# Kernel optimization log

Measured on AMD Instinct MI355X. Metric: run time of the kernel, lower is better.

The kernel has to match this reference:

```python
import jax, jax.numpy as jnp
import numpy as np
from math import pi

N = 20000        # nodes
E = 640000       # edges (avg degree 32)
H = 128          # hidden_channels = num_filters
NB = 3           # num_bond_features
NGS = 50 - NB    # gaussians in smearing (num_gaussians - num_bond_features)
CUT = 10.0       # cutoff
L = 3            # num_interactions
B = 16           # graphs in batch
LOG2 = 0.6931471805599453


def ssp(x):
    # ShiftedSoftplus
    return jax.nn.softplus(x) - LOG2


def setup_inputs() -> dict:
    key = jax.random.key(0)
    ks = jax.random.split(key, 20)
    s = 0.05
    inp = {
        "z": jax.random.randint(ks[0], (N,), 0, 100),
        "pos": jax.random.uniform(ks[1], (N, 3), jnp.float32),
        "batch": jnp.sort(jax.random.randint(ks[2], (N,), 0, B)),
        "edge_index": jax.random.randint(ks[3], (2, E), 0, N),
        "edge_attr": jax.random.uniform(ks[4], (E, NB), jnp.float32),
        # parameters (stacked over L interaction blocks where per-layer)
        "emb": jax.random.normal(ks[5], (100, H), jnp.float32) * s,
        "mlp_w1": jax.random.normal(ks[6], (L, NB + NGS, H), jnp.float32) * s,
        "mlp_b1": jnp.zeros((L, H), jnp.float32),
        "mlp_w2": jax.random.normal(ks[7], (L, H, H), jnp.float32) * s,
        "mlp_b2": jnp.zeros((L, H), jnp.float32),
        "cf1_w": jax.random.normal(ks[8], (L, H, H), jnp.float32) * s,   # lin1, no bias
        "cf2_w": jax.random.normal(ks[9], (L, H, H), jnp.float32) * s,
        "cf2_b": jnp.zeros((L, H), jnp.float32),
        "lin_w": jax.random.normal(ks[10], (L, H, H), jnp.float32) * s,
        "lin_b": jnp.zeros((L, H), jnp.float32),
        "out1_w": jax.random.normal(ks[11], (H, H // 2), jnp.float32) * s,
        "out1_b": jnp.zeros((H // 2,), jnp.float32),
        "out2_w": jax.random.normal(ks[12], (H // 2, 1), jnp.float32) * s,
        "out2_b": jnp.zeros((1,), jnp.float32),
    }
    return inp


def reference(z, pos, batch, edge_index, edge_attr, emb,
              mlp_w1, mlp_b1, mlp_w2, mlp_b2,
              cf1_w, cf2_w, cf2_b, lin_w, lin_b,
              out1_w, out1_b, out2_w, out2_b):
    row, col = edge_index[0], edge_index[1]  # source j, target i
    h = emb[z]                               # [N,H] embedding_e(z)
    # edge_weight = ||pos[row] - pos[col]||
    ew = jnp.linalg.norm(pos[row] - pos[col], axis=-1)  # [E]
    # GaussianSmearing(0, cutoff, NGS)
    offset = jnp.linspace(0.0, CUT, NGS, dtype=jnp.float32)
    coeff = -0.5 / (offset[1] - offset[0]) ** 2
    gs = jnp.exp(coeff * (ew[:, None] - offset[None, :]) ** 2)  # [E,NGS]
    ea = jnp.concatenate([edge_attr, gs], axis=1)  # [E,50]
    # cosine cutoff weight
    C = 0.5 * (jnp.cos(ew * pi / CUT) + 1.0)       # [E]
    for l in range(L):
        # filter MLP on edge features
        W = ssp(ea @ mlp_w1[l] + mlp_b1[l]) @ mlp_w2[l] + mlp_b2[l]  # [E,H]
        W = W * C[:, None]
        xh = h @ cf1_w[l]                    # lin1 (no bias) [N,H]
        msg = xh[row] * W                    # gather-mul [E,H]
        agg = jax.ops.segment_sum(msg, col, num_segments=N)  # scatter-add [N,H]
        xc = agg @ cf2_w[l] + cf2_b[l]       # lin2
        xc = ssp(xc)
        xc = xc @ lin_w[l] + lin_b[l]        # block output lin
        h = h + xc                           # residual
    h = ssp(h @ out1_w + out1_b)             # [N,H/2]
    per_node = h @ out2_w + out2_b           # [N,1]
    out = jax.ops.segment_sum(per_node, batch, num_segments=B)  # readout 'add' -> [B,1]
    return out
```

## Files before the change

kernel.cpp:

```cpp
#include <hip/hip_runtime.h>
#include <hip/hip_bf16.h>

typedef __attribute__((ext_vector_type(8))) short bfrag;
typedef __attribute__((ext_vector_type(4))) float f32x4;

__device__ __forceinline__ float ssp_f(float x) {
    return fmaxf(x, 0.f) + __logf(1.f + __expf(-fabsf(x))) - 0.6931471805599453f;
}

__device__ __forceinline__ unsigned short f2b(float x) {
    __hip_bfloat16 h = __float2bfloat16(x);
    return *(unsigned short*)&h;
}

__global__ void sniff_kernel(const unsigned int* __restrict__ raw, int* __restrict__ flag)
{
    __shared__ int cnt[256];
    const int t = threadIdx.x;
    unsigned int w = raw[t];
    unsigned int e = (w >> 7) & 0xFFu;
    cnt[t] = (e >= 100u && e <= 135u) ? 1 : 0;
    __syncthreads();
    for (int s = 128; s > 0; s >>= 1) {
        if (t < s) cnt[t] += cnt[t + s];
        __syncthreads();
    }
    if (t == 0) *flag = (cnt[0] >= 160) ? 1 : 0;
}

__global__ void sniff_int_kernel(const unsigned int* __restrict__ z, int* __restrict__ iflag)
{
    __shared__ int cnt[128];
    const int t = threadIdx.x;
    cnt[t] = (z[2 * t + 1] == 0u) ? 1 : 0;
    __syncthreads();
    for (int s = 64; s > 0; s >>= 1) {
        if (t < s) cnt[t] += cnt[t + s];
        __syncthreads();
    }
    if (t == 0) *iflag = (cnt[0] >= 126) ? 1 : 0;
}

struct Cvt16 {
    const void* src[16];
    long off[17];
};

__global__ __launch_bounds__(256) void convert_fused_kernel(
    Cvt16 args, float* __restrict__ F, long total, const int* __restrict__ flag)
{
    long i = (long)blockIdx.x * 256 + threadIdx.x;
    if (i >= total) return;
    int lo = 0, hi = 16;
    while (hi - lo > 1) {
        int mid = (lo + hi) >> 1;
        if (i >= args.off[mid]) lo = mid; else hi = mid;
    }
    long loc = i - args.off[lo];
    if (*flag) F[i] = __bfloat162float(((const __hip_bfloat16*)args.src[lo])[loc]);
    else       F[i] = ((const float*)args.src[lo])[loc];
}

__global__ __launch_bounds__(256) void convert_int_kernel(
    const void* __restrict__ src, int* __restrict__ dst, int n,
    const int* __restrict__ iflag)
{
    int i = blockIdx.x * 256 + threadIdx.x;
    if (i >= n) return;
    if (*iflag) dst[i] = (int)(((const long long*)src)[i]);
    else        dst[i] = ((const int*)src)[i];
}

__global__ __launch_bounds__(256) void embed_kernel(
    const int* __restrict__ z, const float* __restrict__ embf,
    float* __restrict__ h, int NH)
{
    int idx = blockIdx.x * 256 + threadIdx.x;
    if (idx >= NH) return;
    h[idx] = embf[z[idx >> 7] * 128 + (idx & 127)];
}

__global__ __launch_bounds__(256) void zero_int_kernel(int* p, int n)
{
    int i = blockIdx.x * 256 + threadIdx.x;
    if (i < n) p[i] = 0;
}

__global__ __launch_bounds__(256) void hist_kernel(const int* __restrict__ col,
                                                   int* __restrict__ count, int E)
{
    int e = blockIdx.x * 256 + threadIdx.x;
    if (e < E) atomicAdd(&count[col[e]], 1);
}

__global__ __launch_bounds__(256) void scan_kernel(const int* __restrict__ count,
                                                   int* __restrict__ rowptr,
                                                   int* __restrict__ next, int N)
{
    __shared__ int part[256];
    const int t = threadIdx.x;
    const int chunk = (N + 255) / 256;
    const int lo = t * chunk, hi = min(lo + chunk, N);
    int s = 0;
    for (int i = lo; i < hi; ++i) s += count[i];
    part[t] = s;
    __syncthreads();
    if (t == 0) {
        int run = 0;
        for (int i = 0; i < 256; ++i) { int v = part[i]; part[i] = run; run += v; }
        rowptr[N] = run;
    }
    __syncthreads();
    int run = part[t];
    for (int i = lo; i < hi; ++i) {
        rowptr[i] = run; next[i] = run;
        run += count[i];
    }
}

__global__ __launch_bounds__(256) void slot_kernel(const int* __restrict__ col,
                                                   int* __restrict__ next,
                                                   int* __restrict__ slot, int E)
{
    int e = blockIdx.x * 256 + threadIdx.x;
    if (e < E) slot[e] = atomicAdd(&next[col[e]], 1);
}

__global__ __launch_bounds__(256) void perm_kernel(const int* __restrict__ slot,
                                                   int* __restrict__ perm, int E)
{
    int e = blockIdx.x * 256 + threadIdx.x;
    if (e < E) perm[slot[e]] = e;
}

__global__ __launch_bounds__(256) void prep_edges_kernel(
    const float* __restrict__ posf, const int* __restrict__ row,
    const int* __restrict__ col, const float* __restrict__ eattrf,
    const int* __restrict__ perm,
    int* __restrict__ rowS, int* __restrict__ colS,
    float* __restrict__ CS, float* __restrict__ ewS,
    unsigned short* __restrict__ eaS, int E, int NB)
{
    int p = blockIdx.x * 256 + threadIdx.x;
    if (p >= E) return;
    const int e = perm[p];
    const int r = row[e], c = col[e];
    float dx = posf[r*3+0] - posf[c*3+0];
    float dy = posf[r*3+1] - posf[c*3+1];
    float dz = posf[r*3+2] - posf[c*3+2];
    float ew = sqrtf(dx*dx + dy*dy + dz*dz);
    rowS[p] = r; colS[p] = c; ewS[p] = ew;
    CS[p] = 0.5f * (cosf(ew * 0.3141592653589793f) + 1.0f);
    unsigned short* o = eaS + (long)p * 4;
    for (int q = 0; q < 4; ++q)
        o[q] = (q < NB) ? f2b(eattrf[(long)e * NB + q]) : (unsigned short)0;
}

__global__ __launch_bounds__(256) void wtrans_kernel(
    const float* __restrict__ src, unsigned short* __restrict__ dst,
    int K, int Kpad, int N)
{
    int idx = blockIdx.x * 256 + threadIdx.x;
    if (idx >= N * Kpad) return;
    int n = idx / Kpad, k = idx - n * Kpad;
    dst[idx] = (k < K) ? f2b(src[k * N + n]) : (unsigned short)0;
}

__global__ __launch_bounds__(256) void wtrans_node_kernel(
    const float* __restrict__ cf1, const float* __restrict__ cf2,
    const float* __restrict__ lin, unsigned short* __restrict__ dst, int total)
{
    int idx = blockIdx.x * 256 + threadIdx.x;
    if (idx >= total) return;
    int m = idx >> 14;
    int fam = m % 3, l = m / 3;
    int local = idx & 16383;
    int n = local >> 7, k = local & 127;
    const float* src = (fam == 0 ? cf1 : fam == 1 ? cf2 : lin) + (long)l * 16384;
    dst[idx] = f2b(src[k * 128 + n]);
}

template<int MODE>
__global__ __launch_bounds__(256) void node_gemm_tiled(
    const float* __restrict__ in, const float* __restrict__ W,
    const float* __restrict__ bias, float* __restrict__ out, int N)
{
    __shared__ float in_s[32][128];
    const int t = threadIdx.x;
    const long n0 = (long)blockIdx.x * 32;
    for (int i = t; i < 32 * 128; i += 256) {
        long n = n0 + (i >> 7);
        in_s[i >> 7][i & 127] = (n < N) ? in[n * 128 + (i & 127)] : 0.f;
    }
    __syncthreads();
    const int j = t & 31, sub = t >> 5;
    const int c4 = j * 4, rb = sub * 4;
    float acc[4][4];
    float4 bv = make_float4(0.f, 0.f, 0.f, 0.f);
    if (MODE != 0) bv = *(const float4*)(bias + c4);
    #pragma unroll
    for (int i = 0; i < 4; ++i) { acc[i][0]=bv.x; acc[i][1]=bv.y; acc[i][2]=bv.z; acc[i][3]=bv.w; }
    #pragma unroll 4
    for (int k = 0; k < 128; ++k) {
        const float4 wv = *(const float4*)(W + k * 128 + c4);
        #pragma unroll
        for (int i = 0; i < 4; ++i) {
            const float a = in_s[rb + i][k];
            acc[i][0] += a * wv.x; acc[i][1] += a * wv.y;
            acc[i][2] += a * wv.z; acc[i][3] += a * wv.w;
        }
    }
    #pragma unroll
    for (int i = 0; i < 4; ++i) {
        long n = n0 + rb + i;
        if (n >= N) continue;
        float4 o;
        if (MODE == 1) {
            o.x = ssp_f(acc[i][0]); o.y = ssp_f(acc[i][1]);
            o.z = ssp_f(acc[i][2]); o.w = ssp_f(acc[i][3]);
        } else {
            o.x = acc[i][0]; o.y = acc[i][1]; o.z = acc[i][2]; o.w = acc[i][3];
        }
        if (MODE == 2) {
            float4 p = *(const float4*)(out + n * 128 + c4);
            o.x += p.x; o.y += p.y; o.z += p.z; o.w += p.w;
        }
        *(float4*)(out + n * 128 + c4) = o;
    }
}

__global__ __launch_bounds__(256) void node_gemm1_mfma(
    const float* __restrict__ in, const unsigned short* __restrict__ wt,
    float* __restrict__ out, int N)
{
    __shared__ __align__(16) short a_b[32][136];
    const int t = threadIdx.x;
    const long r0 = (long)blockIdx.x * 32;
    for (int i = t; i < 32 * 128; i += 256) {
        const int r = i >> 7, c = i & 127;
        long n = r0 + r;
        a_b[r][c] = (short)f2b((n < N) ? in[n * 128 + c] : 0.f);
    }
    __syncthreads();
    const int lane = t & 63, w = t >> 6;
    const int colL = lane & 15, quad = lane >> 4;
    const int m0 = (w & 1) * 16;
    f32x4 acc[4];
    #pragma unroll
    for (int tt = 0; tt < 4; ++tt) acc[tt] = (f32x4){0.f, 0.f, 0.f, 0.f};
    #pragma unroll
    for (int ks = 0; ks < 4; ++ks) {
        const bfrag a = *(const bfrag*)&a_b[m0 + colL][ks * 32 + quad * 8];
        #pragma unroll
        for (int tt = 0; tt < 4; ++tt) {
            const int n0 = ((w >> 1) * 4 + tt) * 16;
            const bfrag b = *(const bfrag*)&wt[(long)(n0 + colL) * 128 + ks * 32 + quad * 8];
            acc[tt] = __builtin_amdgcn_mfma_f32_16x16x32_bf16(a, b, acc[tt], 0, 0, 0);
        }
    }
    #pragma unroll
    for (int tt = 0; tt < 4; ++tt) {
        const int n0 = ((w >> 1) * 4 + tt) * 16;
        #pragma unroll
        for (int reg = 0; reg < 4; ++reg) {
            long n = r0 + m0 + quad * 4 + reg;
            if (n < N) out[n * 128 + n0 + colL] = acc[tt][reg];
        }
    }
}

__global__ __launch_bounds__(256) void node_gemm23_mfma(
    const float* __restrict__ in,
    const unsigned short* __restrict__ w1t, const float* __restrict__ b1,
    const unsigned short* __restrict__ w2t, const float* __restrict__ b2,
    float* __restrict__ h, int N)
{
    __shared__ __align__(16) short a_b[32][136];
    __shared__ __align__(16) short t_b[32][136];
    const int t = threadIdx.x;
    const long r0 = (long)blockIdx.x * 32;
    for (int i = t; i < 32 * 128; i += 256) {
        const int r = i >> 7, c = i & 127;
        long n = r0 + r;
        a_b[r][c] = (short)f2b((n < N) ? in[n * 128 + c] : 0.f);
    }
    __syncthreads();
    const int lane = t & 63, w = t >> 6;
    const int colL = lane & 15, quad = lane >> 4;
    const int m0 = (w & 1) * 16;
    {
        f32x4 acc[4];
        #pragma unroll
        for (int tt = 0; tt < 4; ++tt) acc[tt] = (f32x4){0.f, 0.f, 0.f, 0.f};
        #pragma unroll
        for (int ks = 0; ks < 4; ++ks) {
            const bfrag a = *(const bfrag*)&a_b[m0 + colL][ks * 32 + quad * 8];
            #pragma unroll
            for (int tt = 0; tt < 4; ++tt) {
                const int n0 = ((w >> 1) * 4 + tt) * 16;
                const bfrag b = *(const bfrag*)&w1t[(long)(n0 + colL) * 128 + ks * 32 + quad * 8];
                acc[tt] = __builtin_amdgcn_mfma_f32_16x16x32_bf16(a, b, acc[tt], 0, 0, 0);
            }
        }
        #pragma unroll
        for (int tt = 0; tt < 4; ++tt) {
            const int n0 = ((w >> 1) * 4 + tt) * 16;
            const float bcol = b1[n0 + colL];
            #pragma unroll
            for (int reg = 0; reg < 4; ++reg)
                t_b[m0 + quad * 4 + reg][n0 + colL] = (short)f2b(ssp_f(acc[tt][reg] + bcol));
        }
    }
    __syncthreads();
    {
        f32x4 acc[4];
        #pragma unroll
        for (int tt = 0; tt < 4; ++tt) acc[tt] = (f32x4){0.f, 0.f, 0.f, 0.f};
        #pragma unroll
        for (int ks = 0; ks < 4; ++ks) {
            const bfrag a = *(const bfrag*)&t_b[m0 + colL][ks * 32 + quad * 8];
            #pragma unroll
            for (int tt = 0; tt < 4; ++tt) {
                const int n0 = ((w >> 1) * 4 + tt) * 16;
                const bfrag b = *(const bfrag*)&w2t[(long)(n0 + colL) * 128 + ks * 32 + quad * 8];
                acc[tt] = __builtin_amdgcn_mfma_f32_16x16x32_bf16(a, b, acc[tt], 0, 0, 0);
            }
        }
        #pragma unroll
        for (int tt = 0; tt < 4; ++tt) {
            const int n0 = ((w >> 1) * 4 + tt) * 16;
            const int cg = n0 + colL;
            const float bcol = b2[cg];
            #pragma unroll
            for (int reg = 0; reg < 4; ++reg) {
                long n = r0 + m0 + quad * 4 + reg;
                if (n < N) h[n * 128 + cg] += acc[tt][reg] + bcol;
            }
        }
    }
}

__global__ __launch_bounds__(256, 8) void edge_mfma(
    const int* __restrict__ rowS, const int* __restrict__ colS,
    const float* __restrict__ CS, const float* __restrict__ ewS,
    const unsigned short* __restrict__ eaS,
    const unsigned short* __restrict__ w1t, const float* __restrict__ b1,
    const unsigned short* __restrict__ w2t, const float* __restrict__ b2,
    const float* __restrict__ xh, float* __restrict__ agg,
    int E, int NB, int F50, float delta, float coeff)
{
    __shared__ __align__(16) char smem[32 * 132 * 4];
    short (*ea_b)[64]    = (short(*)[64])smem;
    short (*t_b)[128]    = (short(*)[128])(smem + 4096);
    float (*runbuf)[132] = (float(*)[132])smem;
    __shared__ int   row_s[32];
    __shared__ int   col_s[32];
    __shared__ float C_s[32];
    __shared__ float ew_s[32];

    const int t = threadIdx.x;
    const long p0 = (long)blockIdx.x * 32;

    if (t < 32) {
        long p = p0 + t; if (p >= E) p = E - 1;
        row_s[t] = rowS[p];
        col_s[t] = colS[p];
        C_s[t]   = (p0 + t < E) ? CS[p] : 0.f;
        ew_s[t]  = ewS[p];
    }
    __syncthreads();
    for (int i = t; i < 32 * 64; i += 256) {
        const int e = i >> 6, k = i & 63;
        long p = p0 + e; if (p >= E) p = E - 1;
        unsigned short v;
        if (k < NB)        v = eaS[p * 4 + k];
        else if (k < F50) {
            float d = ew_s[e] - (float)(k - NB) * delta;
            v = f2b(__expf(coeff * d * d));
        } else             v = 0;
        ea_b[e][k ^ ((e & 7) << 3)] = (short)v;
    }
    __syncthreads();

    const int lane = t & 63;
    const int w    = t >> 6;
    const int colL = lane & 15;
    const int quad = lane >> 4;
    const int m0   = (w & 1) * 16;

    {
        f32x4 acc[4];
        #pragma unroll
        for (int tt = 0; tt < 4; ++tt) acc[tt] = (f32x4){0.f, 0.f, 0.f, 0.f};
        const int ar  = m0 + colL;
        const int asw = (ar & 7) << 3;
        #pragma unroll
        for (int ks = 0; ks < 2; ++ks) {
            const bfrag a = *(const bfrag*)&ea_b[ar][(ks * 32 + quad * 8) ^ asw];
            #pragma unroll
            for (int tt = 0; tt < 4; ++tt) {
                const int n0 = ((w >> 1) * 4 + tt) * 16;
                const bfrag b = *(const bfrag*)&w1t[(long)(n0 + colL) * 64 + ks * 32 + quad * 8];
                acc[tt] = __builtin_amdgcn_mfma_f32_16x16x32_bf16(a, b, acc[tt], 0, 0, 0);
            }
        }
        #pragma unroll
        for (int tt = 0; tt < 4; ++tt) {
            const int n0 = ((w >> 1) * 4 + tt) * 16;
            const float bcol = b1[n0 + colL];
            #pragma unroll
            for (int reg = 0; reg < 4; ++reg) {
                const int rr = m0 + quad * 4 + reg;
                float v = ssp_f(acc[tt][reg] + bcol);
                t_b[rr][(n0 + colL) ^ ((rr & 7) << 3)] = (short)f2b(v);
            }
        }
    }
    __syncthreads();

    {
        f32x4 acc[4];
        #pragma unroll
        for (int tt = 0; tt < 4; ++tt) acc[tt] = (f32x4){0.f, 0.f, 0.f, 0.f};
        const int ar  = m0 + colL;
        const int asw = (ar & 7) << 3;
        #pragma unroll
        for (int ks = 0; ks < 4; ++ks) {
            const bfrag a = *(const bfrag*)&t_b[ar][(ks * 32 + quad * 8) ^ asw];
            #pragma unroll
            for (int tt = 0; tt < 4; ++tt) {
                const int n0 = ((w >> 1) * 4 + tt) * 16;
                const bfrag b = *(const bfrag*)&w2t[(long)(n0 + colL) * 128 + ks * 32 + quad * 8];
                acc[tt] = __builtin_amdgcn_mfma_f32_16x16x32_bf16(a, b, acc[tt], 0, 0, 0);
            }
        }
        __syncthreads();
        const int ebase = m0 + quad * 4;
        #pragma unroll
        for (int tt = 0; tt < 4; ++tt) {
            const int n0 = ((w >> 1) * 4 + tt) * 16;
            const int cg = n0 + colL;
            const float bcol = b2[cg];
            #pragma unroll
            for (int reg = 0; reg < 4; ++reg) {
                const int e = ebase + reg;
                const float v = acc[tt][reg] + bcol;
                runbuf[e][cg] = v * C_s[e] * xh[(long)row_s[e] * 128 + cg];
            }
        }
    }
    __syncthreads();

    {
        const int cc   = t & 127;
        const int e0h  = (t >> 7) * 16;
        float a     = runbuf[e0h][cc];
        int  curcol = col_s[e0h];
        #pragma unroll 4
        for (int e = e0h + 1; e < e0h + 16; ++e) {
            const int c2 = col_s[e];
            if (c2 != curcol) {
                atomicAdd(&agg[(long)curcol * 128 + cc], a);
                a = 0.f; curcol = c2;
            }
            a += runbuf[e][cc];
        }
        atomicAdd(&agg[(long)curcol * 128 + cc], a);
    }
}

__global__ __launch_bounds__(256) void edge_atomic(
    const float* __restrict__ posf,
    const int* __restrict__ row, const int* __restrict__ col,
    const float* __restrict__ eattrf,
    const float* __restrict__ w1, const float* __restrict__ b1,
    const float* __restrict__ w2, const float* __restrict__ b2,
    const float* __restrict__ xh, float* __restrict__ agg,
    int E, int NB, int F50, float delta, float coeff)
{
    __shared__ float ea_s[32][52];
    __shared__ float t_s[32][128];
    __shared__ int   row_s[32];
    __shared__ int   col_s[32];
    __shared__ float C_s[32];
    __shared__ float ew_s[32];

    const int t = threadIdx.x;
    const long e0 = (long)blockIdx.x * 32;

    if (t < 32) {
        long e = e0 + t; if (e >= E) e = E - 1;
        const int r = row[e], c = col[e];
        row_s[t] = r; col_s[t] = c;
        float dx = posf[r*3+0] - posf[c*3+0];
        float dy = posf[r*3+1] - posf[c*3+1];
        float dz = posf[r*3+2] - posf[c*3+2];
        float ew = sqrtf(dx*dx + dy*dy + dz*dz);
        ew_s[t] = ew;
        C_s[t]  = (e0 + t < E) ? 0.5f * (cosf(ew * 0.3141592653589793f) + 1.0f) : 0.f;
        for (int q = 0; q < NB; ++q)
            ea_s[t][q] = eattrf[e * NB + q];
    }
    __syncthreads();
    {
        const int NGS = F50 - NB;
        for (int i = t; i < 32 * NGS; i += 256) {
            const int e = i / NGS, g = i - e * NGS;
            const float d = ew_s[e] - (float)g * delta;
            ea_s[e][NB + g] = __expf(coeff * d * d);
        }
    }
    __syncthreads();

    const int j = t & 31, sub = t >> 5;
    const int c4 = j * 4, eb = sub * 4;
    float acc[4][4];
    {
        const float4 bv = *(const float4*)(b1 + c4);
        #pragma unroll
        for (int i = 0; i < 4; ++i) { acc[i][0]=bv.x; acc[i][1]=bv.y; acc[i][2]=bv.z; acc[i][3]=bv.w; }
        for (int k = 0; k < F50; ++k) {
            const float4 wv = *(const float4*)(w1 + k * 128 + c4);
            #pragma unroll
            for (int i = 0; i < 4; ++i) {
                const float a = ea_s[eb + i][k];
                acc[i][0] += a * wv.x; acc[i][1] += a * wv.y;
                acc[i][2] += a * wv.z; acc[i][3] += a * wv.w;
            }
        }
        #pragma unroll
        for (int i = 0; i < 4; ++i) {
            float4 o;
            o.x = ssp_f(acc[i][0]); o.y = ssp_f(acc[i][1]);
            o.z = ssp_f(acc[i][2]); o.w = ssp_f(acc[i][3]);
            *(float4*)&t_s[eb + i][c4] = o;
        }
    }
    __syncthreads();
    {
        const float4 bv = *(const float4*)(b2 + c4);
        #pragma unroll
        for (int i = 0; i < 4; ++i) { acc[i][0]=bv.x; acc[i][1]=bv.y; acc[i][2]=bv.z; acc[i][3]=bv.w; }
        #pragma unroll 4
        for (int k = 0; k < 128; ++k) {
            const float4 wv = *(const float4*)(w2 + k * 128 + c4);
            #pragma unroll
            for (int i = 0; i < 4; ++i) {
                const float a = t_s[eb + i][k];
                acc[i][0] += a * wv.x; acc[i][1] += a * wv.y;
                acc[i][2] += a * wv.z; acc[i][3] += a * wv.w;
            }
        }
    }
    #pragma unroll
    for (int i = 0; i < 4; ++i) {
        const int e = eb + i;
        if (e0 + e >= E) continue;
        const float Ce = C_s[e];
        const float4 xv = *(const float4*)(xh + (long)row_s[e] * 128 + c4);
        float* ag = agg + (long)col_s[e] * 128 + c4;
        atomicAdd(ag + 0, acc[i][0] * Ce * xv.x);
        atomicAdd(ag + 1, acc[i][1] * Ce * xv.y);
        atomicAdd(ag + 2, acc[i][2] * Ce * xv.z);
        atomicAdd(ag + 3, acc[i][3] * Ce * xv.w);
    }
}

__global__ __launch_bounds__(128) void readout_simple(
    const float* __restrict__ h,
    const float* __restrict__ o1w, const float* __restrict__ o1b,
    const float* __restrict__ o2w, const float* __restrict__ o2b,
    const int* __restrict__ batch, float* __restrict__ accb)
{
    __shared__ float hr[128];
    __shared__ float vv[64];
    const int n = blockIdx.x;
    const int t = threadIdx.x;
    hr[t] = h[(long)n * 128 + t];
    __syncthreads();
    if (t < 64) {
        float a = o1b[t];
        #pragma unroll 8
        for (int k = 0; k < 128; ++k)
            a = fmaf(hr[k], o1w[k * 64 + t], a);
        vv[t] = ssp_f(a) * o2w[t];
    }
    __syncthreads();
    if (t < 32) vv[t] += vv[t + 32];
    __syncthreads();
    if (t < 16) vv[t] += vv[t + 16];
    __syncthreads();
    if (t < 8)  vv[t] += vv[t + 8];
    __syncthreads();
    if (t < 4)  vv[t] += vv[t + 4];
    __syncthreads();
    if (t < 2)  vv[t] += vv[t + 2];
    __syncthreads();
    if (t == 0) atomicAdd(&accb[batch[n]], vv[0] + vv[1] + o2b[0]);
}

__global__ void finalize_kernel(const float* __restrict__ accb,
                                float* __restrict__ out, int B)
{
    int t = blockIdx.x * 256 + threadIdx.x;
    if (t < B) out[t] = accb[t];
}

extern "C" void kernel_launch(void* const* d_in, const int* in_sizes, int n_in,
                              void* d_out, int out_size, void* d_ws, size_t ws_size,
                              hipStream_t stream)
{
    const int N   = in_sizes[0];
    const int E   = in_sizes[3] / 2;
    const int B   = out_size;
    const int H   = 128;
    const int L   = in_sizes[7] / H;
    const int NB  = in_sizes[4] / E;
    const int F50 = in_sizes[6] / (L * H);
    const int NGS = F50 - NB;
    const float delta = 10.0f / (float)(NGS - 1);
    const float coeff = -0.5f / (delta * delta);

    const int fidx[16] = {1, 4, 5, 6, 7, 8, 9, 10, 11, 12, 13, 14, 15, 16, 17, 18};
    Cvt16 cv;
    cv.off[0] = 0;
    for (int i = 0; i < 16; ++i) {
        cv.src[i] = d_in[fidx[i]];
        cv.off[i + 1] = cv.off[i] + in_sizes[fidx[i]];
    }
    const long ftot = cv.off[16];

    float* F = (float*)d_ws;
    long base = (ftot + 3) & ~3L;
    float* h    = F + base;
    float* xh   = h + (long)N * H;
    float* agg  = xh + (long)N * H;
    float* accb = agg + (long)N * H;
    int*   flag  = (int*)(accb + ((B + 3) & ~3));
    int*   iflag = flag + 1;
    int*   zi     = flag + 4;
    int*   batchi = zi + N;
    int*   eidxi  = batchi + N;
    int*   count  = eidxi + 2 * E;
    int*   rowptr = count + N;
    int*   next   = rowptr + N + 1;
    int*   slot   = next + N;
    int*   perm   = slot + E;
    int*   rowS   = perm + E;
    int*   colS   = rowS + E;
    float* CS     = (float*)(colS + E);
    float* ewS    = CS + E;
    unsigned short* eaS = (unsigned short*)(ewS + E);
    unsigned short* w1t = eaS + 4L * E;
    unsigned short* w2t = w1t + (long)L * 128 * 64;
    unsigned short* nwt = w2t + (long)L * 128 * 128;
    long used_bytes = (long)((char*)(nwt + 3L * L * 128 * 128) - (char*)d_ws);
    const bool use_fast = (used_bytes <= (long)ws_size) && (F50 <= 64) && (NB <= 4);

    sniff_kernel<<<1, 256, 0, stream>>>((const unsigned int*)d_in[5], flag);
    sniff_int_kernel<<<1, 128, 0, stream>>>((const unsigned int*)d_in[0], iflag);

    convert_fused_kernel<<<(int)((ftot + 255) / 256), 256, 0, stream>>>(cv, F, ftot, flag);
    convert_int_kernel<<<(N + 255) / 256, 256, 0, stream>>>(d_in[0], zi, N, iflag);
    convert_int_kernel<<<(N + 255) / 256, 256, 0, stream>>>(d_in[2], batchi, N, iflag);
    convert_int_kernel<<<(2 * E + 255) / 256, 256, 0, stream>>>(d_in[3], eidxi, 2 * E, iflag);

    const float* posf   = F + cv.off[0];
    const float* eattrf = F + cv.off[1];
    const float* embf   = F + cv.off[2];
    const float* w1   = F + cv.off[3];  const float* b1   = F + cv.off[4];
    const float* w2   = F + cv.off[5];  const float* b2   = F + cv.off[6];
    const float* cf1  = F + cv.off[7];  const float* cf2  = F + cv.off[8];
    const float* cf2b = F + cv.off[9];  const float* lin  = F + cv.off[10];
    const float* linb = F + cv.off[11]; const float* o1   = F + cv.off[12];
    const float* o1b  = F + cv.off[13]; const float* o2   = F + cv.off[14];
    const float* o2b  = F + cv.off[15];

    if (use_fast) {
        zero_int_kernel<<<(N + 255) / 256, 256, 0, stream>>>(count, N);
        hist_kernel<<<(E + 255) / 256, 256, 0, stream>>>(eidxi + E, count, E);
        scan_kernel<<<1, 256, 0, stream>>>(count, rowptr, next, N);
        slot_kernel<<<(E + 255) / 256, 256, 0, stream>>>(eidxi + E, next, slot, E);
        perm_kernel<<<(E + 255) / 256, 256, 0, stream>>>(slot, perm, E);
        prep_edges_kernel<<<(E + 255) / 256, 256, 0, stream>>>(
            posf, eidxi, eidxi + E, eattrf, perm, rowS, colS, CS, ewS, eaS, E, NB);
        for (int l = 0; l < L; ++l) {
            wtrans_kernel<<<(128 * 64 + 255) / 256, 256, 0, stream>>>(
                w1 + (long)l * F50 * H, w1t + (long)l * 128 * 64, F50, 64, 128);
            wtrans_kernel<<<(128 * 128 + 255) / 256, 256, 0, stream>>>(
                w2 + (long)l * H * H, w2t + (long)l * 128 * 128, 128, 128, 128);
        }
        const int ntot = 3 * L * 128 * 128;
        wtrans_node_kernel<<<(ntot + 255) / 256, 256, 0, stream>>>(cf1, cf2, lin, nwt, ntot);
    }

    embed_kernel<<<(N * H + 255) / 256, 256, 0, stream>>>(zi, embf, h, N * H);
    hipMemsetAsync(accb, 0, (size_t)B * sizeof(float), stream);

    const int ngemm = (N + 31) / 32;
    const int nedge = (E + 31) / 32;
    for (int l = 0; l < L; ++l) {
        hipMemsetAsync(agg, 0, (size_t)N * H * sizeof(float), stream);
        if (use_fast) {
            node_gemm1_mfma<<<ngemm, 256, 0, stream>>>(
                h, nwt + (long)(l * 3 + 0) * 16384, xh, N);
            edge_mfma<<<nedge, 256, 0, stream>>>(
                rowS, colS, CS, ewS, eaS,
                w1t + (long)l * 128 * 64, b1 + (long)l * H,
                w2t + (long)l * 128 * 128, b2 + (long)l * H,
                xh, agg, E, NB, F50, delta, coeff);
            node_gemm23_mfma<<<ngemm, 256, 0, stream>>>(
                agg, nwt + (long)(l * 3 + 1) * 16384, cf2b + (long)l * H,
                nwt + (long)(l * 3 + 2) * 16384, linb + (long)l * H, h, N);
        } else {
            node_gemm_tiled<0><<<ngemm, 256, 0, stream>>>(h, cf1 + (long)l * H * H, nullptr, xh, N);
            edge_atomic<<<nedge, 256, 0, stream>>>(
                posf, eidxi, eidxi + E, eattrf,
                w1 + (long)l * F50 * H, b1 + (long)l * H,
                w2 + (long)l * H * H,  b2 + (long)l * H,
                xh, agg, E, NB, F50, delta, coeff);
            node_gemm_tiled<1><<<ngemm, 256, 0, stream>>>(agg, cf2 + (long)l * H * H, cf2b + (long)l * H, xh, N);
            node_gemm_tiled<2><<<ngemm, 256, 0, stream>>>(xh, lin + (long)l * H * H, linb + (long)l * H, h, N);
        }
    }

    readout_simple<<<N, 128, 0, stream>>>(h, o1, o1b, o2, o2b, batchi, accb);
    finalize_kernel<<<(B + 255) / 256, 256, 0, stream>>>(accb, (float*)d_out, B);
}
```

Measured before the change: 1.430 ms.

## Fuse edge prep scatter, zero agg in gemm1, transpose MFMA operands, add MFMA readout

Merges the slot/perm/prep kernels into one atomic-scatter prep kernel. Zeroing of the aggregation buffer moves into the first node GEMM, replacing a separate memset. All MFMA kernels now swap operands so each lane holds four contiguous output columns, which allows float4 stores, packed bf16 staging and vectorised bias loads; the edge kernel also folds the cutoff into the first filter layer. The per-node readout is replaced by a tiled MFMA kernel with a shared-memory reduction. Atomic slot order now depends on scheduling, so the within-segment edge order is nondeterministic.

```diff
diff --git a/kernel.cpp b/kernel.cpp
--- a/kernel.cpp
+++ b/kernel.cpp
@@ -11,6 +11,25 @@
 __device__ __forceinline__ unsigned short f2b(float x) {
     __hip_bfloat16 h = __float2bfloat16(x);
     return *(unsigned short*)&h;
+}
+
+__device__ __forceinline__ unsigned int pk2(float a, float b) {
+    __hip_bfloat162 h2 = __float22bfloat162_rn(make_float2(a, b));
+    return *(unsigned int*)&h2;
+}
+
+__device__ __forceinline__ void stage32x128(
+    const float* __restrict__ src, long r0, int N, int t, short (*dst)[136])
+{
+    #pragma unroll
+    for (int j = 0; j < 4; ++j) {
+        const int fi = t + j * 256;
+        const int r = fi >> 5, c4 = (fi & 31) << 2;
+        const long n = r0 + r;
+        float4 v = make_float4(0.f, 0.f, 0.f, 0.f);
+        if (n < N) v = *(const float4*)(src + n * 128 + c4);
+        *(uint2*)&dst[r][c4] = make_uint2(pk2(v.x, v.y), pk2(v.z, v.w));
+    }
 }
 
 __global__ void sniff_kernel(const unsigned int* __restrict__ raw, int* __restrict__ flag)
@@ -118,33 +137,18 @@
     }
 }
 
-__global__ __launch_bounds__(256) void slot_kernel(const int* __restrict__ col,
-                                                   int* __restrict__ next,
-                                                   int* __restrict__ slot, int E)
-{
-    int e = blockIdx.x * 256 + threadIdx.x;
-    if (e < E) slot[e] = atomicAdd(&next[col[e]], 1);
-}
-
-__global__ __launch_bounds__(256) void perm_kernel(const int* __restrict__ slot,
-                                                   int* __restrict__ perm, int E)
-{
-    int e = blockIdx.x * 256 + threadIdx.x;
-    if (e < E) perm[slot[e]] = e;
-}
-
-__global__ __launch_bounds__(256) void prep_edges_kernel(
+__global__ __launch_bounds__(256) void prep_scatter_kernel(
     const float* __restrict__ posf, const int* __restrict__ row,
     const int* __restrict__ col, const float* __restrict__ eattrf,
-    const int* __restrict__ perm,
+    int* __restrict__ next,
     int* __restrict__ rowS, int* __restrict__ colS,
     float* __restrict__ CS, float* __restrict__ ewS,
     unsigned short* __restrict__ eaS, int E, int NB)
 {
-    int p = blockIdx.x * 256 + threadIdx.x;
-    if (p >= E) return;
-    const int e = perm[p];
+    int e = blockIdx.x * 256 + threadIdx.x;
+    if (e >= E) return;
     const int r = row[e], c = col[e];
+    const int p = atomicAdd(&next[c], 1);
     float dx = posf[r*3+0] - posf[c*3+0];
     float dy = posf[r*3+1] - posf[c*3+1];
     float dz = posf[r*3+2] - posf[c*3+2];
@@ -231,40 +235,45 @@
 
 __global__ __launch_bounds__(256) void node_gemm1_mfma(
     const float* __restrict__ in, const unsigned short* __restrict__ wt,
-    float* __restrict__ out, int N)
+    float* __restrict__ out, float* __restrict__ aggz, int N)
 {
     __shared__ __align__(16) short a_b[32][136];
     const int t = threadIdx.x;
     const long r0 = (long)blockIdx.x * 32;
-    for (int i = t; i < 32 * 128; i += 256) {
-        const int r = i >> 7, c = i & 127;
-        long n = r0 + r;
-        a_b[r][c] = (short)f2b((n < N) ? in[n * 128 + c] : 0.f);
+    stage32x128(in, r0, N, t, a_b);
+    {
+        const float4 z = make_float4(0.f, 0.f, 0.f, 0.f);
+        #pragma unroll
+        for (int j = 0; j < 4; ++j) {
+            const int fi = t + j * 256;
+            const long n = r0 + (fi >> 5);
+            if (n < N) *(float4*)(aggz + n * 128 + ((fi & 31) << 2)) = z;
+        }
     }
     __syncthreads();
     const int lane = t & 63, w = t >> 6;
     const int colL = lane & 15, quad = lane >> 4;
-    const int m0 = (w & 1) * 16;
+    const int rt = (w & 1) * 16 + colL;
+    const int nh = (w >> 1) * 64;
     f32x4 acc[4];
     #pragma unroll
     for (int tt = 0; tt < 4; ++tt) acc[tt] = (f32x4){0.f, 0.f, 0.f, 0.f};
     #pragma unroll
     for (int ks = 0; ks < 4; ++ks) {
-        const bfrag a = *(const bfrag*)&a_b[m0 + colL][ks * 32 + quad * 8];
+        const bfrag a = *(const bfrag*)&a_b[rt][ks * 32 + quad * 8];
         #pragma unroll
         for (int tt = 0; tt < 4; ++tt) {
-            const int n0 = ((w >> 1) * 4 + tt) * 16;
-            const bfrag b = *(const bfrag*)&wt[(long)(n0 + colL) * 128 + ks * 32 + quad * 8];
-            acc[tt] = __builtin_amdgcn_mfma_f32_16x16x32_bf16(a, b, acc[tt], 0, 0, 0);
-        }
-    }
-    #pragma unroll
-    for (int tt = 0; tt < 4; ++tt) {
-        const int n0 = ((w >> 1) * 4 + tt) * 16;
-        #pragma unroll
-        for (int reg = 0; reg < 4; ++reg) {
-            long n = r0 + m0 + quad * 4 + reg;
-            if (n < N) out[n * 128 + n0 + colL] = acc[tt][reg];
+            const bfrag wf = *(const bfrag*)&wt[(long)(nh + tt * 16 + colL) * 128 + ks * 32 + quad * 8];
+            acc[tt] = __builtin_amdgcn_mfma_f32_16x16x32_bf16(wf, a, acc[tt], 0, 0, 0);
+        }
+    }
+    const long node = r0 + rt;
+    if (node < N) {
+        float* orow = out + node * 128;
+        #pragma unroll
+        for (int tt = 0; tt < 4; ++tt) {
+            const int c0 = nh + tt * 16 + quad * 4;
+            *(float4*)(orow + c0) = make_float4(acc[tt][0], acc[tt][1], acc[tt][2], acc[tt][3]);
         }
     }
 }
@@ -279,36 +288,34 @@
     __shared__ __align__(16) short t_b[32][136];
     const int t = threadIdx.x;
     const long r0 = (long)blockIdx.x * 32;
-    for (int i = t; i < 32 * 128; i += 256) {
-        const int r = i >> 7, c = i & 127;
-        long n = r0 + r;
-        a_b[r][c] = (short)f2b((n < N) ? in[n * 128 + c] : 0.f);
-    }
+    stage32x128(in, r0, N, t, a_b);
     __syncthreads();
     const int lane = t & 63, w = t >> 6;
     const int colL = lane & 15, quad = lane >> 4;
-    const int m0 = (w & 1) * 16;
+    const int rt = (w & 1) * 16 + colL;
+    const int nh = (w >> 1) * 64;
     {
         f32x4 acc[4];
         #pragma unroll
         for (int tt = 0; tt < 4; ++tt) acc[tt] = (f32x4){0.f, 0.f, 0.f, 0.f};
         #pragma unroll
         for (int ks = 0; ks < 4; ++ks) {
-            const bfrag a = *(const bfrag*)&a_b[m0 + colL][ks * 32 + quad * 8];
+            const bfrag a = *(const bfrag*)&a_b[rt][ks * 32 + quad * 8];
             #pragma unroll
             for (int tt = 0; tt < 4; ++tt) {
-                const int n0 = ((w >> 1) * 4 + tt) * 16;
-                const bfrag b = *(const bfrag*)&w1t[(long)(n0 + colL) * 128 + ks * 32 + quad * 8];
-                acc[tt] = __builtin_amdgcn_mfma_f32_16x16x32_bf16(a, b, acc[tt], 0, 0, 0);
+                const bfrag wf = *(const bfrag*)&w1t[(long)(nh + tt * 16 + colL) * 128 + ks * 32 + quad * 8];
+                acc[tt] = __builtin_amdgcn_mfma_f32_16x16x32_bf16(wf, a, acc[tt], 0, 0, 0);
             }
         }
         #pragma unroll
         for (int tt = 0; tt < 4; ++tt) {
-            const int n0 = ((w >> 1) * 4 + tt) * 16;
-            const float bcol = b1[n0 + colL];
-            #pragma unroll
-            for (int reg = 0; reg < 4; ++reg)
-                t_b[m0 + quad * 4 + reg][n0 + colL] = (short)f2b(ssp_f(acc[tt][reg] + bcol));
+            const int c0 = nh + tt * 16 + quad * 4;
+            const float4 bv = *(const float4*)(b1 + c0);
+            const float v0 = ssp_f(acc[tt][0] + bv.x);
+            const float v1 = ssp_f(acc[tt][1] + bv.y);
+            const float v2 = ssp_f(acc[tt][2] + bv.z);
+            const float v3 = ssp_f(acc[tt][3] + bv.w);
+            *(uint2*)&t_b[rt][c0] = make_uint2(pk2(v0, v1), pk2(v2, v3));
         }
     }
     __syncthreads();
@@ -318,23 +325,26 @@
         for (int tt = 0; tt < 4; ++tt) acc[tt] = (f32x4){0.f, 0.f, 0.f, 0.f};
         #pragma unroll
         for (int ks = 0; ks < 4; ++ks) {
-            const bfrag a = *(const bfrag*)&t_b[m0 + colL][ks * 32 + quad * 8];
+            const bfrag a = *(const bfrag*)&t_b[rt][ks * 32 + quad * 8];
             #pragma unroll
             for (int tt = 0; tt < 4; ++tt) {
-                const int n0 = ((w >> 1) * 4 + tt) * 16;
-                const bfrag b = *(const bfrag*)&w2t[(long)(n0 + colL) * 128 + ks * 32 + quad * 8];
-                acc[tt] = __builtin_amdgcn_mfma_f32_16x16x32_bf16(a, b, acc[tt], 0, 0, 0);
+                const bfrag wf = *(const bfrag*)&w2t[(long)(nh + tt * 16 + colL) * 128 + ks * 32 + quad * 8];
+                acc[tt] = __builtin_amdgcn_mfma_f32_16x16x32_bf16(wf, a, acc[tt], 0, 0, 0);
             }
         }
-        #pragma unroll
-        for (int tt = 0; tt < 4; ++tt) {
-            const int n0 = ((w >> 1) * 4 + tt) * 16;
-            const int cg = n0 + colL;
-            const float bcol = b2[cg];
+        const long node = r0 + rt;
+        if (node < N) {
+            float* hrow = h + node * 128;
             #pragma unroll
-            for (int reg = 0; reg < 4; ++reg) {
-                long n = r0 + m0 + quad * 4 + reg;
-                if (n < N) h[n * 128 + cg] += acc[tt][reg] + bcol;
+            for (int tt = 0; tt < 4; ++tt) {
+                const int c0 = nh + tt * 16 + quad * 4;
+                const float4 bv = *(const float4*)(b2 + c0);
+                float4 hv = *(const float4*)(hrow + c0);
+                hv.x += acc[tt][0] + bv.x;
+                hv.y += acc[tt][1] + bv.y;
+                hv.z += acc[tt][2] + bv.z;
+                hv.w += acc[tt][3] + bv.w;
+                *(float4*)(hrow + c0) = hv;
             }
         }
     }
@@ -369,16 +379,26 @@
         ew_s[t]  = ewS[p];
     }
     __syncthreads();
-    for (int i = t; i < 32 * 64; i += 256) {
-        const int e = i >> 6, k = i & 63;
+    #pragma unroll
+    for (int j = 0; j < 4; ++j) {
+        const int pi = t + j * 256;
+        const int e  = pi >> 5;
+        const int k0 = (pi & 31) * 2;
         long p = p0 + e; if (p >= E) p = E - 1;
-        unsigned short v;
-        if (k < NB)        v = eaS[p * 4 + k];
-        else if (k < F50) {
-            float d = ew_s[e] - (float)(k - NB) * delta;
-            v = f2b(__expf(coeff * d * d));
-        } else             v = 0;
-        ea_b[e][k ^ ((e & 7) << 3)] = (short)v;
+        const float ew = ew_s[e];
+        float f[2];
+        #pragma unroll
+        for (int q = 0; q < 2; ++q) {
+            const int k = k0 + q;
+            if (k < NB) {
+                unsigned int ui = (unsigned int)eaS[p * 4 + k] << 16;
+                f[q] = *(float*)&ui;
+            } else if (k < F50) {
+                const float d = ew - (float)(k - NB) * delta;
+                f[q] = __expf(coeff * d * d);
+            } else f[q] = 0.f;
+        }
+        *(unsigned int*)&ea_b[e][k0 ^ ((e & 7) << 3)] = pk2(f[0], f[1]);
     }
     __syncthreads();
 
@@ -386,67 +406,67 @@
     const int w    = t >> 6;
     const int colL = lane & 15;
     const int quad = lane >> 4;
-    const int m0   = (w & 1) * 16;
+    const int et   = (w & 1) * 16 + colL;
+    const int nh   = (w >> 1) * 64;
+    const int esw  = (et & 7) << 3;
+    const float Ct = C_s[et];
 
     {
         f32x4 acc[4];
         #pragma unroll
         for (int tt = 0; tt < 4; ++tt) acc[tt] = (f32x4){0.f, 0.f, 0.f, 0.f};
-        const int ar  = m0 + colL;
-        const int asw = (ar & 7) << 3;
         #pragma unroll
         for (int ks = 0; ks < 2; ++ks) {
-            const bfrag a = *(const bfrag*)&ea_b[ar][(ks * 32 + quad * 8) ^ asw];
+            const bfrag ea = *(const bfrag*)&ea_b[et][(ks * 32 + quad * 8) ^ esw];
             #pragma unroll
             for (int tt = 0; tt < 4; ++tt) {
-                const int n0 = ((w >> 1) * 4 + tt) * 16;
-                const bfrag b = *(const bfrag*)&w1t[(long)(n0 + colL) * 64 + ks * 32 + quad * 8];
-                acc[tt] = __builtin_amdgcn_mfma_f32_16x16x32_bf16(a, b, acc[tt], 0, 0, 0);
+                const bfrag wf = *(const bfrag*)&w1t[(long)(nh + tt * 16 + colL) * 64 + ks * 32 + quad * 8];
+                acc[tt] = __builtin_amdgcn_mfma_f32_16x16x32_bf16(wf, ea, acc[tt], 0, 0, 0);
             }
         }
         #pragma unroll
         for (int tt = 0; tt < 4; ++tt) {
-            const int n0 = ((w >> 1) * 4 + tt) * 16;
-            const float bcol = b1[n0 + colL];
-            #pragma unroll
-            for (int reg = 0; reg < 4; ++reg) {
-                const int rr = m0 + quad * 4 + reg;
-                float v = ssp_f(acc[tt][reg] + bcol);
-                t_b[rr][(n0 + colL) ^ ((rr & 7) << 3)] = (short)f2b(v);
-            }
+            const int c0 = nh + tt * 16 + quad * 4;
+            const float4 bv = *(const float4*)(b1 + c0);
+            const float v0 = ssp_f(acc[tt][0] + bv.x) * Ct;
+            const float v1 = ssp_f(acc[tt][1] + bv.y) * Ct;
+            const float v2 = ssp_f(acc[tt][2] + bv.z) * Ct;
+            const float v3 = ssp_f(acc[tt][3] + bv.w) * Ct;
+            *(uint2*)&t_b[et][c0 ^ esw] = make_uint2(pk2(v0, v1), pk2(v2, v3));
         }
     }
     __syncthreads();
 
     {
+        const float* xrow = xh + (long)row_s[et] * 128;
+        const float4 xv0 = *(const float4*)(xrow + nh +  0 + quad * 4);
+        const float4 xv1 = *(const float4*)(xrow + nh + 16 + quad * 4);
+        const float4 xv2 = *(const float4*)(xrow + nh + 32 + quad * 4);
+        const float4 xv3 = *(const float4*)(xrow + nh + 48 + quad * 4);
         f32x4 acc[4];
         #pragma unroll
         for (int tt = 0; tt < 4; ++tt) acc[tt] = (f32x4){0.f, 0.f, 0.f, 0.f};
-        const int ar  = m0 + colL;
-        const int asw = (ar & 7) << 3;
         #pragma unroll
         for (int ks = 0; ks < 4; ++ks) {
-            const bfrag a = *(const bfrag*)&t_b[ar][(ks * 32 + quad * 8) ^ asw];
+            const bfrag tf = *(const bfrag*)&t_b[et][(ks * 32 + quad * 8) ^ esw];
             #pragma unroll
             for (int tt = 0; tt < 4; ++tt) {
-                const int n0 = ((w >> 1) * 4 + tt) * 16;
-                const bfrag b = *(const bfrag*)&w2t[(long)(n0 + colL) * 128 + ks * 32 + quad * 8];
-                acc[tt] = __builtin_amdgcn_mfma_f32_16x16x32_bf16(a, b, acc[tt], 0, 0, 0);
+                const bfrag wf = *(const bfrag*)&w2t[(long)(nh + tt * 16 + colL) * 128 + ks * 32 + quad * 8];
+                acc[tt] = __builtin_amdgcn_mfma_f32_16x16x32_bf16(wf, tf, acc[tt], 0, 0, 0);
             }
         }
         __syncthreads();
-        const int ebase = m0 + quad * 4;
+        const float4 xv[4] = {xv0, xv1, xv2, xv3};
         #pragma unroll
         for (int tt = 0; tt < 4; ++tt) {
-            const int n0 = ((w >> 1) * 4 + tt) * 16;
-            const int cg = n0 + colL;
-            const float bcol = b2[cg];
-            #pragma unroll
-            for (int reg = 0; reg < 4; ++reg) {
-                const int e = ebase + reg;
-                const float v = acc[tt][reg] + bcol;
-                runbuf[e][cg] = v * C_s[e] * xh[(long)row_s[e] * 128 + cg];
-            }
+            const int c0 = nh + tt * 16 + quad * 4;
+            const float4 bv = *(const float4*)(b2 + c0);
+            float4 o;
+            o.x = (acc[tt][0] + Ct * bv.x) * xv[tt].x;
+            o.y = (acc[tt][1] + Ct * bv.y) * xv[tt].y;
+            o.z = (acc[tt][2] + Ct * bv.z) * xv[tt].z;
+            o.w = (acc[tt][3] + Ct * bv.w) * xv[tt].w;
+            *(float4*)&runbuf[et][c0] = o;
         }
     }
     __syncthreads();
@@ -563,6 +583,56 @@
         atomicAdd(ag + 1, acc[i][1] * Ce * xv.y);
         atomicAdd(ag + 2, acc[i][2] * Ce * xv.z);
         atomicAdd(ag + 3, acc[i][3] * Ce * xv.w);
+    }
+}
+
+__global__ __launch_bounds__(256) void readout_mfma(
+    const float* __restrict__ h, const unsigned short* __restrict__ o1t,
+    const float* __restrict__ o1b, const float* __restrict__ o2w,
+    const float* __restrict__ o2b, const int* __restrict__ batch,
+    float* __restrict__ accb, int N)
+{
+    __shared__ __align__(16) short a_b[32][136];
+    __shared__ float nb[32];
+    const int t = threadIdx.x;
+    const long r0 = (long)blockIdx.x * 32;
+    stage32x128(h, r0, N, t, a_b);
+    if (t < 32) nb[t] = 0.f;
+    __syncthreads();
+    const int lane = t & 63, w = t >> 6;
+    const int colL = lane & 15, quad = lane >> 4;
+    const int rt = (w & 1) * 16 + colL;
+    const int nh = (w >> 1) * 32;
+    f32x4 acc[2];
+    #pragma unroll
+    for (int tt = 0; tt < 2; ++tt) acc[tt] = (f32x4){0.f, 0.f, 0.f, 0.f};
+    #pragma unroll
+    for (int ks = 0; ks < 4; ++ks) {
+        const bfrag a = *(const bfrag*)&a_b[rt][ks * 32 + quad * 8];
+        #pragma unroll
+        for (int tt = 0; tt < 2; ++tt) {
+            const bfrag wf = *(const bfrag*)&o1t[(long)(nh + tt * 16 + colL) * 128 + ks * 32 + quad * 8];
+            acc[tt] = __builtin_amdgcn_mfma_f32_16x16x32_bf16(wf, a, acc[tt], 0, 0, 0);
+        }
+    }
+    float s = 0.f;
+    #pragma unroll
+    for (int tt = 0; tt < 2; ++tt) {
+        const int c0 = nh + tt * 16 + quad * 4;
+        const float4 bv = *(const float4*)(o1b + c0);
+        const float4 wv = *(const float4*)(o2w + c0);
+        s += ssp_f(acc[tt][0] + bv.x) * wv.x;
+        s += ssp_f(acc[tt][1] + bv.y) * wv.y;
+        s += ssp_f(acc[tt][2] + bv.z) * wv.z;
+        s += ssp_f(acc[tt][3] + bv.w) * wv.w;
+    }
+    s += __shfl_xor(s, 16);
+    s += __shfl_xor(s, 32);
+    if (quad == 0) atomicAdd(&nb[rt], s);
+    __syncthreads();
+    if (t < 32) {
+        const long node = r0 + t;
+        if (node < N) atomicAdd(&accb[batch[node]], nb[t] + o2b[0]);
     }
 }
 
@@ -644,9 +714,7 @@
     int*   count  = eidxi + 2 * E;
     int*   rowptr = count + N;
     int*   next   = rowptr + N + 1;
-    int*   slot   = next + N;
-    int*   perm   = slot + E;
-    int*   rowS   = perm + E;
+    int*   rowS   = next + N;
     int*   colS   = rowS + E;
     float* CS     = (float*)(colS + E);
     float* ewS    = CS + E;
@@ -654,7 +722,8 @@
     unsigned short* w1t = eaS + 4L * E;
     unsigned short* w2t = w1t + (long)L * 128 * 64;
     unsigned short* nwt = w2t + (long)L * 128 * 128;
-    long used_bytes = (long)((char*)(nwt + 3L * L * 128 * 128) - (char*)d_ws);
+    unsigned short* o1t = nwt + 3L * L * 128 * 128;
+    long used_bytes = (long)((char*)(o1t + 64 * 128) - (char*)d_ws);
     const bool use_fast = (used_bytes <= (long)ws_size) && (F50 <= 64) && (NB <= 4);
 
     sniff_kernel<<<1, 256, 0, stream>>>((const unsigned int*)d_in[5], flag);
@@ -680,10 +749,8 @@
         zero_int_kernel<<<(N + 255) / 256, 256, 0, stream>>>(count, N);
         hist_kernel<<<(E + 255) / 256, 256, 0, stream>>>(eidxi + E, count, E);
         scan_kernel<<<1, 256, 0, stream>>>(count, rowptr, next, N);
-        slot_kernel<<<(E + 255) / 256, 256, 0, stream>>>(eidxi + E, next, slot, E);
-        perm_kernel<<<(E + 255) / 256, 256, 0, stream>>>(slot, perm, E);
-        prep_edges_kernel<<<(E + 255) / 256, 256, 0, stream>>>(
-            posf, eidxi, eidxi + E, eattrf, perm, rowS, colS, CS, ewS, eaS, E, NB);
+        prep_scatter_kernel<<<(E + 255) / 256, 256, 0, stream>>>(
+            posf, eidxi, eidxi + E, eattrf, next, rowS, colS, CS, ewS, eaS, E, NB);
         for (int l = 0; l < L; ++l) {
             wtrans_kernel<<<(128 * 64 + 255) / 256, 256, 0, stream>>>(
                 w1 + (long)l * F50 * H, w1t + (long)l * 128 * 64, F50, 64, 128);
@@ -692,6 +759,7 @@
         }
         const int ntot = 3 * L * 128 * 128;
         wtrans_node_kernel<<<(ntot + 255) / 256, 256, 0, stream>>>(cf1, cf2, lin, nwt, ntot);
+        wtrans_kernel<<<(64 * 128 + 255) / 256, 256, 0, stream>>>(o1, o1t, 128, 128, 64);
     }
 
     embed_kernel<<<(N * H + 255) / 256, 256, 0, stream>>>(zi, embf, h, N * H);
@@ -700,10 +768,9 @@
     const int ngemm = (N + 31) / 32;
     const int nedge = (E + 31) / 32;
     for (int l = 0; l < L; ++l) {
-        hipMemsetAsync(agg, 0, (size_t)N * H * sizeof(float), stream);
         if (use_fast) {
             node_gemm1_mfma<<<ngemm, 256, 0, stream>>>(
-                h, nwt + (long)(l * 3 + 0) * 16384, xh, N);
+                h, nwt + (long)(l * 3 + 0) * 16384, xh, agg, N);
             edge_mfma<<<nedge, 256, 0, stream>>>(
                 rowS, colS, CS, ewS, eaS,
                 w1t + (long)l * 128 * 64, b1 + (long)l * H,
@@ -713,6 +780,7 @@
                 agg, nwt + (long)(l * 3 + 1) * 16384, cf2b + (long)l * H,
                 nwt + (long)(l * 3 + 2) * 16384, linb + (long)l * H, h, N);
         } else {
+            hipMemsetAsync(agg, 0, (size_t)N * H * sizeof(float), stream);
             node_gemm_tiled<0><<<ngemm, 256, 0, stream>>>(h, cf1 + (long)l * H * H, nullptr, xh, N);
             edge_atomic<<<nedge, 256, 0, stream>>>(
                 posf, eidxi, eidxi + E, eattrf,
@@ -724,6 +792,10 @@
         }
     }
 
-    readout_simple<<<N, 128, 0, stream>>>(h, o1, o1b, o2, o2b, batchi, accb);
+    if (use_fast) {
+        readout_mfma<<<ngemm, 256, 0, stream>>>(h, o1t, o1b, o2, o2b, batchi, accb, N);
+    } else {
+        readout_simple<<<N, 128, 0, stream>>>(h, o1, o1b, o2, o2b, batchi, accb);
+    }
     finalize_kernel<<<(B + 255) / 256, 256, 0, stream>>>(accb, (float*)d_out, B);
 }
```

Result: slower. 1.475 ms (+3.2%).
